# Performance work log

Hardware: AMD Instinct MI355X
Metric: run time of the kernel (lower is better)

Reference implementation:

```python
import jax, jax.numpy as jnp
import numpy as np

D = 64; H = 8; HD = 8; L = 3; FFN = 256
MAX_CHUNKS = 1024; MCL = 16


def rms_norm(x, w, eps=1e-6):
    return x * w * jax.lax.rsqrt(jnp.mean(x * x, axis=-1, keepdims=True) + eps)


def rope(x):
    # x: [B, S, H, HD]
    S, hd = x.shape[1], x.shape[-1]
    half = hd // 2
    freqs = 1.0 / (10000.0 ** (jnp.arange(half, dtype=x.dtype) * 2.0 / hd))
    ang = jnp.arange(S, dtype=x.dtype)[:, None] * freqs  # [S, half]
    cos = jnp.cos(ang)[None, :, None, :]
    sin = jnp.sin(ang)[None, :, None, :]
    x1, x2 = x[..., :half], x[..., half:]
    return jnp.concatenate([x1 * cos - x2 * sin, x1 * sin + x2 * cos], axis=-1)


def block(x, wq, wk, wv, wo, g1, g2, w1, w2):
    B, S, _ = x.shape
    h = rms_norm(x, g1)
    q = rope((h @ wq).reshape(B, S, H, HD))
    k = rope((h @ wk).reshape(B, S, H, HD))
    v = (h @ wv).reshape(B, S, H, HD)
    scores = jnp.einsum('bqhd,bkhd->bhqk', q, k) / jnp.sqrt(jnp.asarray(HD, x.dtype))
    causal = jnp.tril(jnp.ones((S, S), dtype=bool))
    scores = jnp.where(causal, scores, jnp.asarray(-1e30, x.dtype))
    attn = jax.nn.softmax(scores, axis=-1)
    o = jnp.einsum('bhqk,bkhd->bqhd', attn, v).reshape(B, S, D)
    x = x + o @ wo
    h2 = rms_norm(x, g2)
    return x + jax.nn.gelu(h2 @ w1, approximate=False) @ w2


def setup_inputs() -> dict:
    key = jax.random.key(0)
    ks = jax.random.split(key, 12)
    B, S = 4, 2048
    s = 1.0 / np.sqrt(D)
    return {
        'x': jax.random.normal(ks[0], (B, S, D), jnp.float32),
        'pad_token_vector': jax.random.normal(ks[1], (D,), jnp.float32),
        'x_ids': jax.random.randint(ks[2], (B, S), 0, 256),
        'pad_token_id': 257,
        'Wq': jax.random.normal(ks[3], (L, D, D), jnp.float32) * s,
        'Wk': jax.random.normal(ks[4], (L, D, D), jnp.float32) * s,
        'Wv': jax.random.normal(ks[5], (L, D, D), jnp.float32) * s,
        'Wo': jax.random.normal(ks[6], (L, D, D), jnp.float32) * s,
        'ln1': jnp.ones((L, D), jnp.float32),
        'ln2': jnp.ones((L, D), jnp.float32),
        'W1': jax.random.normal(ks[7], (L, D, FFN), jnp.float32) * s,
        'W2': jax.random.normal(ks[8], (L, FFN, D), jnp.float32) * (1.0 / np.sqrt(FFN)),
        'Whead': jax.random.normal(ks[9], (D, 2), jnp.float32) * s,
        'bhead': jnp.zeros((2,), jnp.float32),
    }


def reference(x, pad_token_vector, x_ids, pad_token_id, Wq, Wk, Wv, Wo, ln1, ln2, W1, W2, Whead, bhead):
    B, S, _ = x.shape
    h = x
    for l in range(L):
        h = block(h, Wq[l], Wk[l], Wv[l], Wo[l], ln1[l], ln2[l], W1[l], W2[l])
    logits = h @ Whead + bhead  # [B, S, 2]
    end_mask = logits[..., 0] > logits[..., 1]  # [B, S]
    t = jnp.arange(S)
    # fallback: if a row has no end, mark the last position as an end
    has_end = jnp.any(end_mask, axis=-1, keepdims=True)
    end_mask = jnp.where(has_end, end_mask, t[None, :] == S - 1)
    em = end_mask.astype(jnp.int32)
    num_ends = jnp.sum(em, axis=-1)                 # [B] = number of chunks
    chunk_id = jnp.cumsum(em, axis=-1) - em         # exclusive count of prior ends
    prev_end = jnp.concatenate([jnp.ones((B, 1), bool), end_mask[:, :-1]], axis=1)
    start_marker = jnp.where(prev_end, t[None, :], -1)
    start = jax.lax.associative_scan(jnp.maximum, start_marker, axis=-1)  # cummax -> chunk start per token
    pos = t[None, :] - start                        # position within chunk
    valid = (chunk_id < num_ends[:, None]) & (chunk_id < MAX_CHUNKS) & (pos < MCL)
    c_idx = jnp.where(valid, chunk_id, MAX_CHUNKS)  # invalid -> dummy chunk, sliced off
    p_idx = jnp.where(valid, pos, 0)
    b_idx = jnp.arange(B)[:, None]
    out = jnp.broadcast_to(pad_token_vector, (B, MAX_CHUNKS + 1, MCL, D))
    out = out.at[b_idx, c_idx, p_idx].set(h)[:, :MAX_CHUNKS]
    ids = jnp.full((B, MAX_CHUNKS + 1, MCL), pad_token_id, dtype=x_ids.dtype)
    ids = ids.at[b_idx, c_idx, p_idx].set(x_ids)[:, :MAX_CHUNKS]
    reg_term = jnp.mean(logits[..., 1])
    return out, ids, reg_term
```

## Files before the change

kernel.cpp:

```cpp
#include <hip/hip_runtime.h>
#include <math.h>

constexpr int D   = 64;
constexpr int H   = 8;
constexpr int HD  = 8;
constexpr int NL  = 3;
constexpr int FFNx= 256;
constexpr int Bb  = 4;
constexpr int Ss  = 2048;
constexpr int NT  = Bb * Ss;
constexpr int MAXC= 1024;
constexpr int MCL = 16;

constexpr int QW   = 128;
constexpr int CH   = 128;
constexpr int TPB  = 136;
constexpr int BPB  = 68;
constexpr int PBSZ = 1152;

constexpr size_t WX  = 0;
constexpr size_t WQ  = 524288;
constexpr size_t WKV = 2621440;
constexpr size_t WPB = 4194304;
constexpr size_t WL1 = 9764864;
constexpr size_t WEM = WL1 + NT;
constexpr size_t WINV= WEM + NT;
constexpr size_t WCT = WINV + Bb*MAXC*MCL;
constexpr size_t WST = WCT + Ss*4;

constexpr float LOG2E = 1.4426950408889634f;

typedef float v2f  __attribute__((ext_vector_type(2)));
typedef float f16v __attribute__((ext_vector_type(16)));
using ckv_t = const __attribute__((address_space(4))) f16v*;

__device__ __forceinline__ float rdlane(float v, int l) {
    return __builtin_bit_cast(float, __builtin_amdgcn_readlane(__builtin_bit_cast(int, v), l));
}

__global__ void k_init(const float* __restrict__ x, float* __restrict__ X,
                       float* __restrict__ ct, float* __restrict__ st) {
    int i = blockIdx.x * blockDim.x + threadIdx.x;
    constexpr int N4 = NT * D / 4;
    if (i < N4) ((float4*)X)[i] = ((const float4*)x)[i];
    if (i < Ss * 4) {
        int s = i >> 2, f = i & 3;
        const float fr[4] = {1.0f, 0.1f, 0.01f, 0.001f};
        float ang = (float)s * fr[f];
        ct[i] = cosf(ang);
        st[i] = sinf(ang);
    }
}

__global__ __launch_bounds__(256) void k_qkv(
    const float* __restrict__ X, const float* __restrict__ Wq,
    const float* __restrict__ Wk, const float* __restrict__ Wv,
    const float* __restrict__ g1, const float* __restrict__ ct,
    const float* __restrict__ st, float* __restrict__ Q,
    float* __restrict__ KV) {
    __shared__ float wq_s[D*D], wk_s[D*D], wv_s[D*D];
    __shared__ float g_s[D];
    int tid = threadIdx.x;
    for (int i = tid; i < D*D; i += 256) {
        wq_s[i] = Wq[i]; wk_s[i] = Wk[i]; wv_s[i] = Wv[i];
    }
    if (tid < D) g_s[tid] = g1[tid];
    __syncthreads();
    int w = tid >> 6, d = tid & 63;
    int t0 = blockIdx.x * 16;
    for (int it = 0; it < 4; ++it) {
        int t = t0 + it*4 + w;
        float xv = X[t*D + d];
        float ss = xv * xv;
        #pragma unroll
        for (int off = 32; off; off >>= 1) ss += __shfl_xor(ss, off);
        float r = 1.0f / sqrtf(ss * (1.0f/D) + 1e-6f);
        float h = xv * g_s[d] * r;
        float aq = 0.f, ak = 0.f, av = 0.f;
        #pragma unroll
        for (int j = 0; j < D; ++j) {
            float hj = rdlane(h, j);
            aq += hj * wq_s[j*D + d];
            ak += hj * wk_s[j*D + d];
            av += hj * wv_s[j*D + d];
        }
        int s  = t & (Ss - 1);
        int e  = d & 7;
        int fi = e & 3;
        float c  = ct[s*4 + fi];
        float sn = st[s*4 + fi];
        float pq = __shfl_xor(aq, 4);
        float pk = __shfl_xor(ak, 4);
        float rq, rk;
        if (e < 4) { rq = aq*c - pq*sn; rk = ak*c - pk*sn; }
        else       { rq = pq*sn + aq*c; rk = pk*sn + ak*c; }
        Q[t*D + d] = rq;
        int bq = t >> 11;
        int hh = d >> 3;
        float* kvp = KV + ((((size_t)(bq*H + hh))*Ss + s) << 4);
        kvp[e]     = rk;
        kvp[8 + e] = av;
    }
}

template<bool DIAG>
__device__ __forceinline__ void attn_loop(
    ckv_t kvs, int L, int rel0,
    const v2f* __restrict__ q01, v2f& l01, v2f* __restrict__ oP) {
    #pragma unroll 4
    for (int j = 0; j < 64; ++j) {
        f16v kv = kvs[j];
        v2f acc;
        acc  = q01[0] * (v2f){kv[0], kv[0]};
        acc += q01[1] * (v2f){kv[1], kv[1]};
        acc += q01[2] * (v2f){kv[2], kv[2]};
        acc += q01[3] * (v2f){kv[3], kv[3]};
        acc += q01[4] * (v2f){kv[4], kv[4]};
        acc += q01[5] * (v2f){kv[5], kv[5]};
        acc += q01[6] * (v2f){kv[6], kv[6]};
        acc += q01[7] * (v2f){kv[7], kv[7]};
        if (DIAG) {
            int rel = rel0 + j;
            if (rel > L)      acc.x = -1e30f;
            if (rel > L + 64) acc.y = -1e30f;
        }
        v2f p;
        p.x = __builtin_amdgcn_exp2f(acc.x);
        p.y = __builtin_amdgcn_exp2f(acc.y);
        l01 += p;
        oP[0] += p * (v2f){kv[8],  kv[8]};
        oP[1] += p * (v2f){kv[9],  kv[9]};
        oP[2] += p * (v2f){kv[10], kv[10]};
        oP[3] += p * (v2f){kv[11], kv[11]};
        oP[4] += p * (v2f){kv[12], kv[12]};
        oP[5] += p * (v2f){kv[13], kv[13]};
        oP[6] += p * (v2f){kv[14], kv[14]};
        oP[7] += p * (v2f){kv[15], kv[15]};
    }
}

__global__ __launch_bounds__(256) void k_attn2(
    const float* __restrict__ Qg, const float* __restrict__ KV,
    float* __restrict__ PB) {
    __shared__ float comb[2][PBSZ];
    int xcd  = blockIdx.x & 7;
    int slot = blockIdx.x >> 3;
    int bhg  = slot / BPB;
    int blk  = slot - bhg * BPB;
    int bh   = bhg * 8 + xcd;
    int wvu  = __builtin_amdgcn_readfirstlane(threadIdx.x >> 6);
    int pair = wvu >> 1;
    int half = wvu & 1;
    int widb = blk * 2 + pair;
    int L = threadIdx.x & 63;
    int rem = widb;
    int s = 0;
    while (rem >= 16 - s) { rem -= 16 - s; ++s; }
    int t = s + rem;
    int b = bh >> 3, h = bh & 7;
    int qmin = t * QW;
    int k0 = s * CH + half * 64;

    const float SC = 0.35355339059327373f * LOG2E;
    const float* qp = Qg + ((size_t)(b*Ss + qmin + L))*D + h*HD;
    float4 qa0 = *(const float4*)(qp);
    float4 qb0 = *(const float4*)(qp + 4);
    float4 qa1 = *(const float4*)(qp + 64*D);
    float4 qb1 = *(const float4*)(qp + 64*D + 4);
    v2f q01[8];
    q01[0] = (v2f){qa0.x*SC, qa1.x*SC};
    q01[1] = (v2f){qa0.y*SC, qa1.y*SC};
    q01[2] = (v2f){qa0.z*SC, qa1.z*SC};
    q01[3] = (v2f){qa0.w*SC, qa1.w*SC};
    q01[4] = (v2f){qb0.x*SC, qb1.x*SC};
    q01[5] = (v2f){qb0.y*SC, qb1.y*SC};
    q01[6] = (v2f){qb0.z*SC, qb1.z*SC};
    q01[7] = (v2f){qb0.w*SC, qb1.w*SC};

    v2f l01 = (v2f){0.f, 0.f};
    v2f oP[8];
    #pragma unroll
    for (int e = 0; e < 8; ++e) oP[e] = (v2f){0.f, 0.f};

    ckv_t kvs = (ckv_t)(unsigned long long)(KV + (((size_t)bh*Ss + k0) << 4));
    if (s == t) attn_loop<true >(kvs, L, half*64, q01, l01, oP);
    else        attn_loop<false>(kvs, L, half*64, q01, l01, oP);

    if (half == 1) {
        comb[pair][L]      = l01.x;
        comb[pair][64 + L] = l01.y;
        #pragma unroll
        for (int e = 0; e < 8; ++e) {
            comb[pair][128 + e*128 + L]      = oP[e].x;
            comb[pair][128 + e*128 + 64 + L] = oP[e].y;
        }
    }
    __syncthreads();
    if (half == 0) {
        float* pb = PB + ((size_t)bh * TPB + widb) * PBSZ;
        pb[L]      = l01.x + comb[pair][L];
        pb[64 + L] = l01.y + comb[pair][64 + L];
        #pragma unroll
        for (int e = 0; e < 8; ++e) {
            pb[128 + e*128 + L]      = oP[e].x + comb[pair][128 + e*128 + L];
            pb[128 + e*128 + 64 + L] = oP[e].y + comb[pair][128 + e*128 + 64 + L];
        }
    }
}

__global__ __launch_bounds__(256) void k_combo(
    const float* __restrict__ PB, float* __restrict__ X,
    const float* __restrict__ Wo) {
    __shared__ float wo_s[D*D];
    __shared__ float oT[32][65];
    int tid = threadIdx.x;
    int seg = blockIdx.x & 3;
    int t   = (blockIdx.x >> 2) & 15;
    int b   = blockIdx.x >> 6;
    for (int i = tid; i < D*D; i += 256) wo_s[i] = Wo[i];

    int h  = tid >> 5;
    int ql = tid & 31;
    int qs = seg*32 + ql;
    int bh = b*8 + h;
    float Lx = 0.f;
    float O[8] = {0,0,0,0,0,0,0,0};
    for (int s3 = 0; s3 <= t; ++s3) {
        int idx = 16*s3 - (s3*(s3-1))/2 + (t - s3);
        const float* pb = PB + (size_t)(bh*TPB + idx) * PBSZ;
        Lx += pb[qs];
        #pragma unroll
        for (int e = 0; e < 8; ++e) O[e] += pb[128 + e*128 + qs];
    }
    float inv = 1.0f / Lx;
    #pragma unroll
    for (int e = 0; e < 8; ++e) oT[ql][h*8 + e] = O[e] * inv;
    __syncthreads();

    int d = tid & 63, wv = tid >> 6;
    #pragma unroll 2
    for (int k = 0; k < 8; ++k) {
        int tt = wv*8 + k;
        float a = 0.f;
        #pragma unroll
        for (int j = 0; j < D; ++j) a += oT[tt][j] * wo_s[j*D + d];
        X[((size_t)(b*Ss) + t*128 + seg*32 + tt)*D + d] += a;
    }
}

template<bool HEAD>
__global__ __launch_bounds__(256) void k_ffn(
    float* __restrict__ X, const float* __restrict__ g2,
    const float* __restrict__ W1, const float* __restrict__ W2,
    const float* __restrict__ Wh, const float* __restrict__ bhp,
    float* __restrict__ logit1, int* __restrict__ em) {
    __shared__ __align__(16) float h2t[64][20];
    __shared__ float part[16][16];
    __shared__ float g_s[D];
    __shared__ __align__(16) float ult[FFNx][20];
    __shared__ float red[4][16][D];
    int tid = threadIdx.x;
    if (tid < D) g_s[tid] = g2[tid];
    int t0 = blockIdx.x * 16;
    int tk = tid >> 4, li = tid & 15;
    float x0 = X[(t0+tk)*D + li];
    float x1 = X[(t0+tk)*D + li + 16];
    float x2 = X[(t0+tk)*D + li + 32];
    float x3 = X[(t0+tk)*D + li + 48];
    part[tk][li] = x0*x0 + x1*x1 + x2*x2 + x3*x3;
    __syncthreads();
    if (tid < 16) {
        float s = 0.f;
        #pragma unroll
        for (int i = 0; i < 16; ++i) s += part[tid][i];
        part[tid][0] = 1.0f / sqrtf(s * (1.0f/D) + 1e-6f);
    }
    __syncthreads();
    float r = part[tk][0];
    h2t[li][tk]      = x0 * g_s[li]      * r;
    h2t[li + 16][tk] = x1 * g_s[li + 16] * r;
    h2t[li + 32][tk] = x2 * g_s[li + 32] * r;
    h2t[li + 48][tk] = x3 * g_s[li + 48] * r;
    __syncthreads();
    {
        int f = tid;
        v2f acc2[8];
        #pragma unroll
        for (int i = 0; i < 8; ++i) acc2[i] = (v2f){0.f, 0.f};
        for (int j = 0; j < D; ++j) {
            float wv = W1[j*FFNx + f];
            v2f wv2 = (v2f){wv, wv};
            const float4* hp = (const float4*)&h2t[j][0];
            float4 a0 = hp[0], a1 = hp[1], a2 = hp[2], a3 = hp[3];
            const v2f* a0v = (const v2f*)&a0;
            const v2f* a1v = (const v2f*)&a1;
            const v2f* a2v = (const v2f*)&a2;
            const v2f* a3v = (const v2f*)&a3;
            acc2[0] += a0v[0]*wv2;  acc2[1] += a0v[1]*wv2;
            acc2[2] += a1v[0]*wv2;  acc2[3] += a1v[1]*wv2;
            acc2[4] += a2v[0]*wv2;  acc2[5] += a2v[1]*wv2;
            acc2[6] += a3v[0]*wv2;  acc2[7] += a3v[1]*wv2;
        }
        #pragma unroll
        for (int i = 0; i < 8; ++i) {
            float ua = acc2[i].x;
            float ub = acc2[i].y;
            ua = 0.5f * ua * (1.0f + erff(ua * 0.70710678118654752f));
            ub = 0.5f * ub * (1.0f + erff(ub * 0.70710678118654752f));
            ult[f][2*i]     = ua;
            ult[f][2*i + 1] = ub;
        }
    }
    __syncthreads();
    {
        int d = tid & 63, fp = tid >> 6;
        v2f acc2[8];
        #pragma unroll
        for (int i = 0; i < 8; ++i) acc2[i] = (v2f){0.f, 0.f};
        for (int fo = 0; fo < 64; ++fo) {
            int f = fp*64 + fo;
            float wv = W2[f*D + d];
            v2f wv2 = (v2f){wv, wv};
            const float4* up = (const float4*)&ult[f][0];
            float4 u0 = up[0], u1 = up[1], u2 = up[2], u3 = up[3];
            const v2f* u0v = (const v2f*)&u0;
            const v2f* u1v = (const v2f*)&u1;
            const v2f* u2v = (const v2f*)&u2;
            const v2f* u3v = (const v2f*)&u3;
            acc2[0] += u0v[0]*wv2;  acc2[1] += u0v[1]*wv2;
            acc2[2] += u1v[0]*wv2;  acc2[3] += u1v[1]*wv2;
            acc2[4] += u2v[0]*wv2;  acc2[5] += u2v[1]*wv2;
            acc2[6] += u3v[0]*wv2;  acc2[7] += u3v[1]*wv2;
        }
        #pragma unroll
        for (int i = 0; i < 8; ++i) {
            red[fp][2*i][d]     = acc2[i].x;
            red[fp][2*i + 1][d] = acc2[i].y;
        }
        __syncthreads();
        int tk2 = tid >> 6;
        #pragma unroll
        for (int k = 0; k < 4; ++k) {
            int tt = tk2 + k*4;
            float sum = red[0][tt][d] + red[1][tt][d] + red[2][tt][d] + red[3][tt][d];
            float xf = X[(t0 + tt)*D + d] + sum;
            X[(t0 + tt)*D + d] = xf;
            if (HEAD) {
                float p0 = xf * Wh[d*2];
                float p1 = xf * Wh[d*2 + 1];
                #pragma unroll
                for (int off = 32; off; off >>= 1) {
                    p0 += __shfl_xor(p0, off);
                    p1 += __shfl_xor(p1, off);
                }
                if (d == 0) {
                    float l0 = p0 + bhp[0], l1 = p1 + bhp[1];
                    em[t0 + tt] = (l0 > l1) ? 1 : 0;
                    logit1[t0 + tt] = l1;
                }
            }
        }
    }
}

__global__ void k_reg(const float* __restrict__ logit1, float* __restrict__ outreg) {
    __shared__ float red[256];
    int tid = threadIdx.x;
    float s = 0.f;
    for (int i = tid; i < NT; i += 256) s += logit1[i];
    red[tid] = s;
    __syncthreads();
    for (int off = 128; off; off >>= 1) {
        if (tid < off) red[tid] += red[tid + off];
        __syncthreads();
    }
    if (tid == 0) *outreg = red[0] * (1.0f / NT);
}

__global__ __launch_bounds__(256) void k_scan(const int* __restrict__ em,
                                              int* __restrict__ inv) {
    __shared__ int ssum[256], smax[256];
    __shared__ int sany, stot;
    int b = blockIdx.x, tid = threadIdx.x;
    int* invb = inv + b * (MAXC*MCL);
    for (int i = tid; i < MAXC*MCL; i += 256) invb[i] = -1;
    __syncthreads();
    const int* e = em + b*Ss;
    int base = tid * 8;
    int loc[8];
    int lsum = 0, lor = 0;
    #pragma unroll
    for (int i = 0; i < 8; ++i) { loc[i] = e[base + i]; lsum += loc[i]; lor |= loc[i]; }
    ssum[tid] = lor;
    __syncthreads();
    if (tid == 0) { int a = 0; for (int i = 0; i < 256; ++i) a |= ssum[i]; sany = a; }
    __syncthreads();
    int any = sany;
    __syncthreads();
    if (!any && tid == 255) { loc[7] = 1; lsum = 1; }
    int prev = (tid == 0) ? 1 : e[base - 1];
    if (!any && tid) prev = 0;
    int mk[8];
    int lmax = -1;
    #pragma unroll
    for (int i = 0; i < 8; ++i) {
        int pe = (i == 0) ? prev : loc[i - 1];
        if (i == 7 && !any && tid == 255) pe = e[base + 6];
        mk[i] = pe ? (base + i) : -1;
        lmax = max(lmax, mk[i]);
    }
    ssum[tid] = lsum; smax[tid] = lmax;
    __syncthreads();
    if (tid == 0) {
        int rs = 0, rm = -1;
        for (int i = 0; i < 256; ++i) {
            int ts = ssum[i], tm = smax[i];
            ssum[i] = rs; smax[i] = rm;
            rs += ts; rm = max(rm, tm);
        }
        stot = rs;
    }
    __syncthreads();
    int run = ssum[tid], rmax = smax[tid], tot = stot;
    #pragma unroll
    for (int i = 0; i < 8; ++i) {
        int s = base + i;
        rmax = max(rmax, mk[i]);
        int chunk = run;
        run += loc[i];
        int pos = s - rmax;
        bool valid = (chunk < tot) && (chunk < MAXC) && (pos < MCL);
        if (valid) invb[chunk * MCL + pos] = b*Ss + s;
    }
}

__global__ __launch_bounds__(256) void k_out(
    const float* __restrict__ X, const float* __restrict__ pad,
    const int* __restrict__ xids, const int* __restrict__ padid,
    const int* __restrict__ inv, float* __restrict__ out) {
    int i = blockIdx.x * blockDim.x + threadIdx.x;
    constexpr int NV4 = Bb * MAXC * MCL * D / 4;
    constexpr int NI4 = Bb * MAXC * MCL / 4;
    if (i < NV4) {
        int slot = i >> 4;
        int d4 = i & 15;
        int t = inv[slot];
        float4 v = (t >= 0) ? ((const float4*)X)[t*16 + d4]
                            : ((const float4*)pad)[d4];
        ((float4*)out)[i] = v;
    } else if (i < NV4 + NI4) {
        int j = i - NV4;
        float pv = (float)(*padid);
        int base = j * 4;
        int t0_ = inv[base], t1_ = inv[base+1], t2_ = inv[base+2], t3_ = inv[base+3];
        float4 v;
        v.x = (t0_ >= 0) ? (float)xids[t0_] : pv;
        v.y = (t1_ >= 0) ? (float)xids[t1_] : pv;
        v.z = (t2_ >= 0) ? (float)xids[t2_] : pv;
        v.w = (t3_ >= 0) ? (float)xids[t3_] : pv;
        ((float4*)out)[i] = v;
    }
}

extern "C" void kernel_launch(void* const* d_in, const int* in_sizes, int n_in,
                              void* d_out, int out_size, void* d_ws, size_t ws_size,
                              hipStream_t stream) {
    const float* x    = (const float*)d_in[0];
    const float* pad  = (const float*)d_in[1];
    const int*   xids = (const int*)  d_in[2];
    const int*   padid= (const int*)  d_in[3];
    const float* Wq   = (const float*)d_in[4];
    const float* Wk   = (const float*)d_in[5];
    const float* Wv   = (const float*)d_in[6];
    const float* Wo   = (const float*)d_in[7];
    const float* ln1  = (const float*)d_in[8];
    const float* ln2  = (const float*)d_in[9];
    const float* W1   = (const float*)d_in[10];
    const float* W2   = (const float*)d_in[11];
    const float* Wh   = (const float*)d_in[12];
    const float* bh   = (const float*)d_in[13];
    float* out = (float*)d_out;
    float* ws  = (float*)d_ws;

    float* X  = ws + WX;
    float* Qb = ws + WQ;
    float* KVb= ws + WKV;
    float* PBb= ws + WPB;
    float* L1b= ws + WL1;
    int*   EMb= (int*)(ws + WEM);
    int*   INVb=(int*)(ws + WINV);
    float* ct = ws + WCT;
    float* st = ws + WST;

    k_init<<<2048, 256, 0, stream>>>(x, X, ct, st);
    for (int l = 0; l < NL; ++l) {
        k_qkv <<<512, 256, 0, stream>>>(X, Wq + l*D*D, Wk + l*D*D, Wv + l*D*D,
                                        ln1 + l*D, ct, st, Qb, KVb);
        k_attn2<<<32*BPB, 256, 0, stream>>>(Qb, KVb, PBb);
        k_combo<<<256, 256, 0, stream>>>(PBb, X, Wo + l*D*D);
        if (l == NL - 1)
            k_ffn<true ><<<NT/16, 256, 0, stream>>>(X, ln2 + l*D, W1 + l*D*FFNx,
                                                    W2 + l*FFNx*D, Wh, bh, L1b, EMb);
        else
            k_ffn<false><<<NT/16, 256, 0, stream>>>(X, ln2 + l*D, W1 + l*D*FFNx,
                                                    W2 + l*FFNx*D, nullptr, nullptr,
                                                    nullptr, nullptr);
    }
    k_reg <<<1, 256, 0, stream>>>(L1b, out + (size_t)Bb*MAXC*MCL*D + Bb*MAXC*MCL);
    k_scan<<<Bb, 256, 0, stream>>>(EMb, INVb);
    k_out <<<(Bb*MAXC*MCL*D/4 + Bb*MAXC*MCL/4 + 255)/256, 256, 0, stream>>>(
        X, pad, xids, padid, INVb, out);
}
```

Before: 282.0 us.

## Widen attention query tile to 256 rows so each KV load serves four queries per lane

Each attention wave now handles 256 query rows (four per lane) instead of 128, so every K/V vector read is reused across twice as many queries. Work items become (query tile, 128-key chunk) pairs with a new triangular indexing. The diagonal handling splits into two mask variants, and on the second diagonal chunk the lower query pair is skipped entirely. The partial-buffer layout and the combine kernel change to match. This doubles the accumulator registers per thread, which may lower occupancy, and it halves the number of work items, which may reduce parallelism.

```diff
diff --git a/kernel.cpp b/kernel.cpp
--- a/kernel.cpp
+++ b/kernel.cpp
@@ -12,11 +12,9 @@
 constexpr int MAXC= 1024;
 constexpr int MCL = 16;
 
-constexpr int QW   = 128;
-constexpr int CH   = 128;
-constexpr int TPB  = 136;
-constexpr int BPB  = 68;
-constexpr int PBSZ = 1152;
+constexpr int TPB  = 72;
+constexpr int BPB  = 36;
+constexpr int PBSZ = 2304;
 
 constexpr size_t WX  = 0;
 constexpr size_t WQ  = 524288;
@@ -103,39 +101,68 @@
     }
 }
 
-template<bool DIAG>
-__device__ __forceinline__ void attn_loop(
+template<int DIAG>
+__device__ __forceinline__ void attn_loop4(
     ckv_t kvs, int L, int rel0,
-    const v2f* __restrict__ q01, v2f& l01, v2f* __restrict__ oP) {
+    const v2f* __restrict__ qp0, const v2f* __restrict__ qp1,
+    v2f& l0, v2f& l1, v2f* __restrict__ o0, v2f* __restrict__ o1) {
     #pragma unroll 4
     for (int j = 0; j < 64; ++j) {
         f16v kv = kvs[j];
-        v2f acc;
-        acc  = q01[0] * (v2f){kv[0], kv[0]};
-        acc += q01[1] * (v2f){kv[1], kv[1]};
-        acc += q01[2] * (v2f){kv[2], kv[2]};
-        acc += q01[3] * (v2f){kv[3], kv[3]};
-        acc += q01[4] * (v2f){kv[4], kv[4]};
-        acc += q01[5] * (v2f){kv[5], kv[5]};
-        acc += q01[6] * (v2f){kv[6], kv[6]};
-        acc += q01[7] * (v2f){kv[7], kv[7]};
-        if (DIAG) {
+        v2f a1;
+        a1  = qp1[0] * (v2f){kv[0], kv[0]};
+        a1 += qp1[1] * (v2f){kv[1], kv[1]};
+        a1 += qp1[2] * (v2f){kv[2], kv[2]};
+        a1 += qp1[3] * (v2f){kv[3], kv[3]};
+        a1 += qp1[4] * (v2f){kv[4], kv[4]};
+        a1 += qp1[5] * (v2f){kv[5], kv[5]};
+        a1 += qp1[6] * (v2f){kv[6], kv[6]};
+        a1 += qp1[7] * (v2f){kv[7], kv[7]};
+        if (DIAG == 2) {
             int rel = rel0 + j;
-            if (rel > L)      acc.x = -1e30f;
-            if (rel > L + 64) acc.y = -1e30f;
-        }
-        v2f p;
-        p.x = __builtin_amdgcn_exp2f(acc.x);
-        p.y = __builtin_amdgcn_exp2f(acc.y);
-        l01 += p;
-        oP[0] += p * (v2f){kv[8],  kv[8]};
-        oP[1] += p * (v2f){kv[9],  kv[9]};
-        oP[2] += p * (v2f){kv[10], kv[10]};
-        oP[3] += p * (v2f){kv[11], kv[11]};
-        oP[4] += p * (v2f){kv[12], kv[12]};
-        oP[5] += p * (v2f){kv[13], kv[13]};
-        oP[6] += p * (v2f){kv[14], kv[14]};
-        oP[7] += p * (v2f){kv[15], kv[15]};
+            if (rel > L)      a1.x = -1e30f;
+            if (rel > L + 64) a1.y = -1e30f;
+        }
+        v2f p1;
+        p1.x = __builtin_amdgcn_exp2f(a1.x);
+        p1.y = __builtin_amdgcn_exp2f(a1.y);
+        l1 += p1;
+        o1[0] += p1 * (v2f){kv[8],  kv[8]};
+        o1[1] += p1 * (v2f){kv[9],  kv[9]};
+        o1[2] += p1 * (v2f){kv[10], kv[10]};
+        o1[3] += p1 * (v2f){kv[11], kv[11]};
+        o1[4] += p1 * (v2f){kv[12], kv[12]};
+        o1[5] += p1 * (v2f){kv[13], kv[13]};
+        o1[6] += p1 * (v2f){kv[14], kv[14]};
+        o1[7] += p1 * (v2f){kv[15], kv[15]};
+        if (DIAG != 2) {
+            v2f a0;
+            a0  = qp0[0] * (v2f){kv[0], kv[0]};
+            a0 += qp0[1] * (v2f){kv[1], kv[1]};
+            a0 += qp0[2] * (v2f){kv[2], kv[2]};
+            a0 += qp0[3] * (v2f){kv[3], kv[3]};
+            a0 += qp0[4] * (v2f){kv[4], kv[4]};
+            a0 += qp0[5] * (v2f){kv[5], kv[5]};
+            a0 += qp0[6] * (v2f){kv[6], kv[6]};
+            a0 += qp0[7] * (v2f){kv[7], kv[7]};
+            if (DIAG == 1) {
+                int rel = rel0 + j;
+                if (rel > L)      a0.x = -1e30f;
+                if (rel > L + 64) a0.y = -1e30f;
+            }
+            v2f p0;
+            p0.x = __builtin_amdgcn_exp2f(a0.x);
+            p0.y = __builtin_amdgcn_exp2f(a0.y);
+            l0 += p0;
+            o0[0] += p0 * (v2f){kv[8],  kv[8]};
+            o0[1] += p0 * (v2f){kv[9],  kv[9]};
+            o0[2] += p0 * (v2f){kv[10], kv[10]};
+            o0[3] += p0 * (v2f){kv[11], kv[11]};
+            o0[4] += p0 * (v2f){kv[12], kv[12]};
+            o0[5] += p0 * (v2f){kv[13], kv[13]};
+            o0[6] += p0 * (v2f){kv[14], kv[14]};
+            o0[7] += p0 * (v2f){kv[15], kv[15]};
+        }
     }
 }
 
@@ -155,11 +182,11 @@
     int L = threadIdx.x & 63;
     int rem = widb;
     int s = 0;
-    while (rem >= 16 - s) { rem -= 16 - s; ++s; }
-    int t = s + rem;
+    while (rem >= 8 - (s >> 1)) { rem -= 8 - (s >> 1); ++s; }
+    int t = (s >> 1) + rem;
     int b = bh >> 3, h = bh & 7;
-    int qmin = t * QW;
-    int k0 = s * CH + half * 64;
+    int qmin = t * 256;
+    int k0 = s * 128 + half * 64;
 
     const float SC = 0.35355339059327373f * LOG2E;
     const float* qp = Qg + ((size_t)(b*Ss + qmin + L))*D + h*HD;
@@ -167,43 +194,57 @@
     float4 qb0 = *(const float4*)(qp + 4);
     float4 qa1 = *(const float4*)(qp + 64*D);
     float4 qb1 = *(const float4*)(qp + 64*D + 4);
-    v2f q01[8];
-    q01[0] = (v2f){qa0.x*SC, qa1.x*SC};
-    q01[1] = (v2f){qa0.y*SC, qa1.y*SC};
-    q01[2] = (v2f){qa0.z*SC, qa1.z*SC};
-    q01[3] = (v2f){qa0.w*SC, qa1.w*SC};
-    q01[4] = (v2f){qb0.x*SC, qb1.x*SC};
-    q01[5] = (v2f){qb0.y*SC, qb1.y*SC};
-    q01[6] = (v2f){qb0.z*SC, qb1.z*SC};
-    q01[7] = (v2f){qb0.w*SC, qb1.w*SC};
-
-    v2f l01 = (v2f){0.f, 0.f};
-    v2f oP[8];
+    float4 qa2 = *(const float4*)(qp + 128*D);
+    float4 qb2 = *(const float4*)(qp + 128*D + 4);
+    float4 qa3 = *(const float4*)(qp + 192*D);
+    float4 qb3 = *(const float4*)(qp + 192*D + 4);
+    v2f qp0[8], qp1[8];
+    qp0[0] = (v2f){qa0.x*SC, qa1.x*SC};  qp1[0] = (v2f){qa2.x*SC, qa3.x*SC};
+    qp0[1] = (v2f){qa0.y*SC, qa1.y*SC};  qp1[1] = (v2f){qa2.y*SC, qa3.y*SC};
+    qp0[2] = (v2f){qa0.z*SC, qa1.z*SC};  qp1[2] = (v2f){qa2.z*SC, qa3.z*SC};
+    qp0[3] = (v2f){qa0.w*SC, qa1.w*SC};  qp1[3] = (v2f){qa2.w*SC, qa3.w*SC};
+    qp0[4] = (v2f){qb0.x*SC, qb1.x*SC};  qp1[4] = (v2f){qb2.x*SC, qb3.x*SC};
+    qp0[5] = (v2f){qb0.y*SC, qb1.y*SC};  qp1[5] = (v2f){qb2.y*SC, qb3.y*SC};
+    qp0[6] = (v2f){qb0.z*SC, qb1.z*SC};  qp1[6] = (v2f){qb2.z*SC, qb3.z*SC};
+    qp0[7] = (v2f){qb0.w*SC, qb1.w*SC};  qp1[7] = (v2f){qb2.w*SC, qb3.w*SC};
+
+    v2f l0 = (v2f){0.f, 0.f}, l1 = (v2f){0.f, 0.f};
+    v2f o0[8], o1[8];
     #pragma unroll
-    for (int e = 0; e < 8; ++e) oP[e] = (v2f){0.f, 0.f};
+    for (int e = 0; e < 8; ++e) { o0[e] = (v2f){0.f, 0.f}; o1[e] = (v2f){0.f, 0.f}; }
 
     ckv_t kvs = (ckv_t)(unsigned long long)(KV + (((size_t)bh*Ss + k0) << 4));
-    if (s == t) attn_loop<true >(kvs, L, half*64, q01, l01, oP);
-    else        attn_loop<false>(kvs, L, half*64, q01, l01, oP);
+    if (s == 2*t)          attn_loop4<1>(kvs, L, half*64, qp0, qp1, l0, l1, o0, o1);
+    else if (s == 2*t + 1) attn_loop4<2>(kvs, L, half*64, qp0, qp1, l0, l1, o0, o1);
+    else                   attn_loop4<0>(kvs, L, half*64, qp0, qp1, l0, l1, o0, o1);
 
     if (half == 1) {
-        comb[pair][L]      = l01.x;
-        comb[pair][64 + L] = l01.y;
+        comb[pair][L]       = l0.x;
+        comb[pair][64 + L]  = l0.y;
+        comb[pair][128 + L] = l1.x;
+        comb[pair][192 + L] = l1.y;
         #pragma unroll
         for (int e = 0; e < 8; ++e) {
-            comb[pair][128 + e*128 + L]      = oP[e].x;
-            comb[pair][128 + e*128 + 64 + L] = oP[e].y;
+            comb[pair][256 + e*256 + L]       = o0[e].x;
+            comb[pair][256 + e*256 + 64 + L]  = o0[e].y;
+            comb[pair][256 + e*256 + 128 + L] = o1[e].x;
+            comb[pair][256 + e*256 + 192 + L] = o1[e].y;
         }
     }
     __syncthreads();
     if (half == 0) {
-        float* pb = PB + ((size_t)bh * TPB + widb) * PBSZ;
-        pb[L]      = l01.x + comb[pair][L];
-        pb[64 + L] = l01.y + comb[pair][64 + L];
+        int pbidx = t*(t+1) + s;
+        float* pb = PB + ((size_t)bh * TPB + pbidx) * PBSZ;
+        pb[L]       = l0.x + comb[pair][L];
+        pb[64 + L]  = l0.y + comb[pair][64 + L];
+        pb[128 + L] = l1.x + comb[pair][128 + L];
+        pb[192 + L] = l1.y + comb[pair][192 + L];
         #pragma unroll
         for (int e = 0; e < 8; ++e) {
-            pb[128 + e*128 + L]      = oP[e].x + comb[pair][128 + e*128 + L];
-            pb[128 + e*128 + 64 + L] = oP[e].y + comb[pair][128 + e*128 + 64 + L];
+            pb[256 + e*256 + L]       = o0[e].x + comb[pair][256 + e*256 + L];
+            pb[256 + e*256 + 64 + L]  = o0[e].y + comb[pair][256 + e*256 + 64 + L];
+            pb[256 + e*256 + 128 + L] = o1[e].x + comb[pair][256 + e*256 + 128 + L];
+            pb[256 + e*256 + 192 + L] = o1[e].y + comb[pair][256 + e*256 + 192 + L];
         }
     }
 }
@@ -214,8 +255,8 @@
     __shared__ float wo_s[D*D];
     __shared__ float oT[32][65];
     int tid = threadIdx.x;
-    int seg = blockIdx.x & 3;
-    int t   = (blockIdx.x >> 2) & 15;
+    int seg = blockIdx.x & 7;
+    int t   = (blockIdx.x >> 3) & 7;
     int b   = blockIdx.x >> 6;
     for (int i = tid; i < D*D; i += 256) wo_s[i] = Wo[i];
 
@@ -223,14 +264,15 @@
     int ql = tid & 31;
     int qs = seg*32 + ql;
     int bh = b*8 + h;
+    int nch = 2*(t+1);
     float Lx = 0.f;
     float O[8] = {0,0,0,0,0,0,0,0};
-    for (int s3 = 0; s3 <= t; ++s3) {
-        int idx = 16*s3 - (s3*(s3-1))/2 + (t - s3);
+    for (int s3 = 0; s3 < nch; ++s3) {
+        int idx = t*(t+1) + s3;
         const float* pb = PB + (size_t)(bh*TPB + idx) * PBSZ;
         Lx += pb[qs];
         #pragma unroll
-        for (int e = 0; e < 8; ++e) O[e] += pb[128 + e*128 + qs];
+        for (int e = 0; e < 8; ++e) O[e] += pb[256 + e*256 + qs];
     }
     float inv = 1.0f / Lx;
     #pragma unroll
@@ -244,7 +286,7 @@
         float a = 0.f;
         #pragma unroll
         for (int j = 0; j < D; ++j) a += oT[tt][j] * wo_s[j*D + d];
-        X[((size_t)(b*Ss) + t*128 + seg*32 + tt)*D + d] += a;
+        X[((size_t)(b*Ss) + t*256 + seg*32 + tt)*D + d] += a;
     }
 }
 
```

Result: no change. 281.8 us (-0.1%).
